# Performance work log

Hardware: AMD Instinct MI355X
Metric: run time of the kernel (lower is better)

The kernel has to match this reference:

```python
import jax, jax.numpy as jnp
import numpy as np

T_MAX = 0.3  # clamp ceiling for effective opacity (t_max init kwarg)


def setup_inputs() -> dict:
    key = jax.random.key(0)
    k0, k1, k2 = jax.random.split(key, 3)
    B, n_blobs, d_s, d_f = 1024, 131072, 64, 256
    return {
        "query": jax.random.normal(k0, (B, d_s), dtype=jnp.float32),
        "mu": jax.random.normal(k1, (n_blobs, d_s), dtype=jnp.float32) * 0.02,
        "log_var": jnp.zeros((n_blobs, d_s), dtype=jnp.float32),
        "raw_alpha": jnp.zeros((n_blobs,), dtype=jnp.float32),
        "features": jax.random.normal(k2, (n_blobs, d_f), dtype=jnp.float32) * 0.02,
        "log_tau": jnp.asarray(np.log(128.0), dtype=jnp.float32),
        "k": 16,
    }


def reference(query, mu, log_var, raw_alpha, features, log_tau, k):
    # query: [B, d_s]; mu/log_var: [N, d_s]; features: [N, d_f]
    tau = jnp.exp(log_tau)
    inv_var = jnp.exp(-log_var)                              # [N, d_s]
    # Mahalanobis distance expanded to avoid the [B, N, d_s] diff tensor:
    # sum_d (q - mu)^2 * iv = q^2.iv - 2 q.(mu*iv) + sum(mu^2*iv)
    q2 = jnp.einsum('bd,nd->bn', query * query, inv_var)      # [B, N]
    cross = jnp.einsum('bd,nd->bn', query, mu * inv_var)      # [B, N]
    m2 = jnp.sum(mu * mu * inv_var, axis=-1)                  # [N]
    mahal = q2 - 2.0 * cross + m2[None, :]
    K_all = jnp.exp(-0.5 * mahal / tau)                       # [B, N]
    alpha = jax.nn.sigmoid(raw_alpha)                         # [N]
    scores = K_all * alpha[None, :]
    top_scores, top_idx = jax.lax.top_k(scores, k)            # [B, k]

    # Gather selected blobs and recompute exact kernel (as in the original render)
    blob_feats = features[top_idx]                            # [B, k, d_f]
    blob_mu = mu[top_idx]                                     # [B, k, d_s]
    blob_iv = jnp.exp(-log_var[top_idx])                      # [B, k, d_s]
    diff = query[:, None, :] - blob_mu                        # [B, k, d_s]
    mahal_k = jnp.sum(diff * diff * blob_iv, axis=-1)         # [B, k]
    K_topk = jnp.exp(-0.5 * mahal_k / tau)
    blob_alpha = alpha[top_idx]                               # [B, k]

    # Alpha compositing in log space
    eff = jnp.minimum(blob_alpha * K_topk, T_MAX / k)         # [B, k]
    log_1m = jnp.log1p(-jnp.minimum(eff, 1.0 - 1e-6))
    log_cum = jnp.cumsum(log_1m, axis=-1)
    log_T = jnp.concatenate(
        [jnp.zeros_like(log_cum[:, :1]), log_cum[:, :-1]], axis=-1)
    weights = eff * jnp.exp(log_T)                            # [B, k]
    blob_meaning = jnp.einsum('bk,bkd->bd', weights, blob_feats)  # [B, d_f]
    t_residual = jnp.exp(log_cum[:, -1])                      # [B]
    return blob_meaning, t_residual
```

## Files before the change

kernel.cpp:

```cpp
#include <hip/hip_runtime.h>
#include <math.h>

#define BQ    1024
#define NB    131072
#define DS    64
#define DF    256
#define KSEL  16

#define QT    128
#define BC    64
#define PCH   64
#define NCHUNK (NB / BC)
#define CHUNKS_PER_BLK (NCHUNK/PCH)
#define CPQ   (PCH * KSEL)
#define SLD   68

#define CH_BYTES   32768
#define SPLIT_OFF  16384

typedef __bf16 bf16x8 __attribute__((ext_vector_type(8)));
typedef float  f32x4  __attribute__((ext_vector_type(4)));
typedef unsigned long long u64;

__device__ __forceinline__ unsigned map_f32(float s) {
    unsigned u = __float_as_uint(s);
    return (u & 0x80000000u) ? ~u : (u | 0x80000000u);
}

__device__ __forceinline__ void async_cp16(const void* g, void* l) {
    __builtin_amdgcn_global_load_lds(
        (const __attribute__((address_space(1))) unsigned int*)g,
        (__attribute__((address_space(3))) unsigned int*)l, 16, 0, 0);
}

__global__ __launch_bounds__(256)
void prep_kernel(const float* __restrict__ mu,
                 const float* __restrict__ log_var,
                 const float* __restrict__ raw_alpha,
                 char* __restrict__ bprep,
                 float* __restrict__ m2la)
{
    int gid  = blockIdx.x * 256 + threadIdx.x;
    int blob = gid >> 3;
    int dd   = gid & 7;

    const float* mrow = mu      + (size_t)blob * DS + dd * 8;
    const float* vrow = log_var + (size_t)blob * DS + dd * 8;
    float4 ma = ((const float4*)mrow)[0], mb = ((const float4*)mrow)[1];
    float4 va = ((const float4*)vrow)[0], vb = ((const float4*)vrow)[1];
    float m[8] = {ma.x, ma.y, ma.z, ma.w, mb.x, mb.y, mb.z, mb.w};
    float lv[8] = {va.x, va.y, va.z, va.w, vb.x, vb.y, vb.z, vb.w};

    bf16x8 hiv, liv, hmv, lmv;
    float p = 0.0f;
    #pragma unroll
    for (int j = 0; j < 8; ++j) {
        float iv = __expf(-lv[j]);
        float mv = m[j] * iv;
        p += m[j] * mv;
        __bf16 h1 = (__bf16)iv;  hiv[j] = h1; liv[j] = (__bf16)(iv - (float)h1);
        __bf16 h2 = (__bf16)mv;  hmv[j] = h2; lmv[j] = (__bf16)(mv - (float)h2);
    }
    p += __shfl_xor(p, 1);
    p += __shfl_xor(p, 2);
    p += __shfl_xor(p, 4);

    int c  = blob >> 6;
    int nt = (blob >> 4) & 3;
    int bl = blob & 15;
    int lane  = (dd & 3) * 16 + bl;
    int ks_iv = dd >> 2;
    int ks_mv = 2 + (dd >> 2);
    size_t b_iv = (size_t)c * CH_BYTES + nt * 4096 + ks_iv * 1024 + lane * 16;
    size_t b_mv = (size_t)c * CH_BYTES + nt * 4096 + ks_mv * 1024 + lane * 16;
    *(bf16x8*)(bprep + b_iv)             = hiv;
    *(bf16x8*)(bprep + b_iv + SPLIT_OFF) = liv;
    *(bf16x8*)(bprep + b_mv)             = hmv;
    *(bf16x8*)(bprep + b_mv + SPLIT_OFF) = lmv;

    if (dd == 0) {
        m2la[blob * 2]     = p;
        m2la[blob * 2 + 1] = -log1pf(__expf(-raw_alpha[blob]));
    }
}

__device__ __forceinline__ void ins16(float (&ts)[16], int (&ti)[16],
                                      float& mymin, float s, int idx)
{
    float v0[8]; int j0[8];
    #pragma unroll
    for (int i = 0; i < 8; ++i) {
        bool b = ts[2*i+1] < ts[2*i];
        v0[i] = b ? ts[2*i+1] : ts[2*i];
        j0[i] = (i << 1) | (b ? 1 : 0);
    }
    float v1[4]; int j1[4];
    #pragma unroll
    for (int i = 0; i < 4; ++i) {
        bool b = v0[2*i+1] < v0[2*i];
        v1[i] = b ? v0[2*i+1] : v0[2*i];
        j1[i] = b ? j0[2*i+1] : j0[2*i];
    }
    float v2[2]; int j2[2];
    #pragma unroll
    for (int i = 0; i < 2; ++i) {
        bool b = v1[2*i+1] < v1[2*i];
        v2[i] = b ? v1[2*i+1] : v1[2*i];
        j2[i] = b ? j1[2*i+1] : j1[2*i];
    }
    int am = (v2[1] < v2[0]) ? j2[1] : j2[0];
    #pragma unroll
    for (int i = 0; i < 16; ++i) {
        bool b = (i == am);
        ts[i] = b ? s : ts[i];
        ti[i] = b ? idx : ti[i];
    }
    float n0[8];
    #pragma unroll
    for (int i = 0; i < 8; ++i) n0[i] = fminf(ts[2*i], ts[2*i+1]);
    float n1[4];
    #pragma unroll
    for (int i = 0; i < 4; ++i) n1[i] = fminf(n0[2*i], n0[2*i+1]);
    mymin = fminf(fminf(n1[0], n1[1]), fminf(n1[2], n1[3]));
}

__global__ __launch_bounds__(256, 2)
void score_topk_kernel(const float* __restrict__ query,
                       const char* __restrict__ bprep,
                       const float* __restrict__ m2la,
                       const float* __restrict__ log_tau_p,
                       u64* __restrict__ cand)
{
    __shared__ __align__(16) short Bs[CH_BYTES / 2];
    __shared__ __align__(16) float St[QT * SLD];
    __shared__ float scv[2 * QT];

    const int tid   = threadIdx.x;
    const int lane  = tid & 63;
    const int quad  = lane >> 4;
    const int mrow  = lane & 15;
    const int wv    = tid >> 6;
    const int qbase = blockIdx.y * QT;

    const float nhit = -0.5f * expf(-log_tau_p[0]);

    bf16x8 ahi[2][4], alo[2][4];
    #pragma unroll
    for (int mt = 0; mt < 2; ++mt) {
        const float* qrow = query + (size_t)(qbase + wv * 32 + mt * 16 + mrow) * DS;
        #pragma unroll
        for (int ks = 0; ks < 4; ++ks) {
            int kq = ks * 32 + quad * 8;
            int d0 = kq & 63;
            bool lin = kq >= 64;
            bf16x8 h, l;
            #pragma unroll
            for (int j = 0; j < 8; ++j) {
                float v = qrow[d0 + j];
                float x = lin ? (-2.0f * v) : (v * v);
                __bf16 hb = (__bf16)x;
                h[j] = hb;
                l[j] = (__bf16)(x - (float)hb);
            }
            ahi[mt][ks] = h; alo[mt][ks] = l;
        }
    }

    float ts[16]; int ti[16];
    #pragma unroll
    for (int i = 0; i < 16; ++i) { ts[i] = -INFINITY; ti[i] = 0; }
    float mymin = -INFINITY;
    const int qloc = tid & 127;
    const int half = tid >> 7;
    if (tid < 2 * QT) scv[tid] = -INFINITY;

    const char* BsB = (const char*)Bs;

    int c = blockIdx.x;
    {
        const char* src = bprep + (size_t)c * CH_BYTES;
        #pragma unroll
        for (int i = 0; i < 8; ++i) {
            int s = tid + i * 256;
            async_cp16(src + s * 16, (void*)(BsB + s * 16));
        }
    }
    __syncthreads();

    for (int it = 0; it < CHUNKS_PER_BLK; ++it) {
        const int nbase = c * BC;
        const int cn    = c + PCH;
        const bool more = (it + 1) < CHUNKS_PER_BLK;

        float2 ml[4];
        #pragma unroll
        for (int nt = 0; nt < 4; ++nt)
            ml[nt] = *(const float2*)&m2la[(size_t)(nbase + nt * 16 + mrow) * 2];

        f32x4 acc[2][4];
        #pragma unroll
        for (int nt = 0; nt < 4; ++nt) {
            bf16x8 bh[4], bl[4];
            #pragma unroll
            for (int ks = 0; ks < 4; ++ks) {
                bh[ks] = *(const bf16x8*)(BsB + nt * 4096 + ks * 1024 + lane * 16);
                bl[ks] = *(const bf16x8*)(BsB + SPLIT_OFF + nt * 4096 + ks * 1024 + lane * 16);
            }
            #pragma unroll
            for (int mt = 0; mt < 2; ++mt) {
                f32x4 a = {0.0f, 0.0f, 0.0f, 0.0f};
                #pragma unroll
                for (int ks = 0; ks < 4; ++ks) {
                    a = __builtin_amdgcn_mfma_f32_16x16x32_bf16(ahi[mt][ks], bh[ks], a, 0, 0, 0);
                    a = __builtin_amdgcn_mfma_f32_16x16x32_bf16(ahi[mt][ks], bl[ks], a, 0, 0, 0);
                    a = __builtin_amdgcn_mfma_f32_16x16x32_bf16(alo[mt][ks], bh[ks], a, 0, 0, 0);
                }
                acc[mt][nt] = a;
            }
        }
        __syncthreads();

        if (more) {
            const char* src = bprep + (size_t)cn * CH_BYTES;
            #pragma unroll
            for (int i = 0; i < 8; ++i) {
                int s = tid + i * 256;
                async_cp16(src + s * 16, (void*)(BsB + s * 16));
            }
        }

        #pragma unroll
        for (int mt = 0; mt < 2; ++mt)
            #pragma unroll
            for (int nt = 0; nt < 4; ++nt) {
                float m2 = ml[nt].x, la = ml[nt].y;
                #pragma unroll
                for (int reg = 0; reg < 4; ++reg) {
                    float sc = nhit * (acc[mt][nt][reg] + m2) + la;
                    St[(wv * 32 + mt * 16 + quad * 4 + reg) * SLD + nt * 16 + mrow] = sc;
                }
            }
        __syncthreads();

        {
            volatile float* vsc = scv;
            float ocut = vsc[(half ^ 1) * QT + qloc];
            float cut = fmaxf(mymin, ocut);
            const float* rowp = &St[qloc * SLD + half * 32];
            unsigned gm = 0u;
            #pragma unroll
            for (int i = 0; i < 8; ++i) {
                float4 v = ((const float4*)rowp)[i];
                float mx = fmaxf(fmaxf(v.x, v.y), fmaxf(v.z, v.w));
                if (mx > cut) gm |= (1u << i);
            }
            while (__any(gm != 0u)) {
                if (gm) {
                    int i = __ffs(gm) - 1;
                    gm &= gm - 1u;
                    float4 v = ((const float4*)rowp)[i];
                    int b0 = nbase + half * 32 + i * 4;
                    if (v.x > cut) { ins16(ts, ti, mymin, v.x, b0);     cut = fmaxf(mymin, ocut); }
                    if (v.y > cut) { ins16(ts, ti, mymin, v.y, b0 + 1); cut = fmaxf(mymin, ocut); }
                    if (v.z > cut) { ins16(ts, ti, mymin, v.z, b0 + 2); cut = fmaxf(mymin, ocut); }
                    if (v.w > cut) { ins16(ts, ti, mymin, v.w, b0 + 3); cut = fmaxf(mymin, ocut); }
                }
            }
            vsc[half * QT + qloc] = mymin;
        }
        __syncthreads();
        c = cn;
    }
    __syncthreads();

    u64* SK = (u64*)St;
    #pragma unroll
    for (int i = 0; i < 16; ++i)
        SK[qloc * 33 + half * 16 + i] =
            ((u64)map_f32(ts[i]) << 32) | (u64)(0xFFFFFFFFu - (unsigned)ti[i]);
    __syncthreads();

    if (tid < QT) {
        u64* row = SK + tid * 33;
        u64* dst = cand + (size_t)(qbase + tid) * CPQ + blockIdx.x * KSEL;
        for (int r = 0; r < KSEL; ++r) {
            int bm = 0; u64 bv = row[0];
            #pragma unroll 4
            for (int j = 1; j < 32; ++j) { u64 v = row[j]; if (v > bv) { bv = v; bm = j; } }
            row[bm] = 0;
            dst[r] = bv;
        }
    }
}

__global__ __launch_bounds__(256)
void merge_composite_kernel(const float* __restrict__ query,
                            const float* __restrict__ mu,
                            const float* __restrict__ log_var,
                            const float* __restrict__ raw_alpha,
                            const float* __restrict__ features,
                            const float* __restrict__ log_tau_p,
                            const u64* __restrict__ cand,
                            float* __restrict__ out)
{
    const int q   = blockIdx.x;
    const int tid = threadIdx.x;
    const int wv = tid >> 6, lane = tid & 63;

    __shared__ u64   wtop[4 * KSEL];
    __shared__ int   sel[KSEL];
    __shared__ float w_sh[KSEL];
    __shared__ float mah[KSEL];
    __shared__ float alp[KSEL];

    u64 k[4];
    #pragma unroll
    for (int r = 0; r < 4; ++r)
        k[r] = cand[(size_t)q * CPQ + wv * 256 + r * 64 + lane];

    for (int r = 0; r < KSEL; ++r) {
        u64 m = k[0];
        #pragma unroll
        for (int j = 1; j < 4; ++j) if (k[j] > m) m = k[j];
        #pragma unroll
        for (int off = 32; off > 0; off >>= 1) {
            unsigned hi = __shfl_xor((unsigned)(m >> 32), off);
            unsigned lo = __shfl_xor((unsigned)(m & 0xFFFFFFFFu), off);
            u64 o = ((u64)hi << 32) | lo;
            if (o > m) m = o;
        }
        if (lane == 0) wtop[wv * KSEL + r] = m;
        #pragma unroll
        for (int j = 0; j < 4; ++j) if (k[j] == m) k[j] = 0ull;
    }
    __syncthreads();

    if (wv == 0) {
        u64 kk = wtop[lane];
        for (int r = 0; r < KSEL; ++r) {
            u64 m = kk;
            #pragma unroll
            for (int off = 32; off > 0; off >>= 1) {
                unsigned hi = __shfl_xor((unsigned)(m >> 32), off);
                unsigned lo = __shfl_xor((unsigned)(m & 0xFFFFFFFFu), off);
                u64 o = ((u64)hi << 32) | lo;
                if (o > m) m = o;
            }
            if (kk == m) kk = 0ull;
            if (lane == 0)
                sel[r] = (int)(0xFFFFFFFFu - (unsigned)(m & 0xFFFFFFFFull));
        }
    }
    __syncthreads();

    for (int r = wv; r < KSEL; r += 4) {
        int bi = sel[r];
        float qd = query[(size_t)q * DS + lane];
        float mv = mu[(size_t)bi * DS + lane];
        float d  = qd - mv;
        float t  = d * d * expf(-log_var[(size_t)bi * DS + lane]);
        #pragma unroll
        for (int off = 32; off > 0; off >>= 1) t += __shfl_down(t, off);
        if (lane == 0) {
            mah[r] = t;
            alp[r] = 1.0f / (1.0f + expf(-raw_alpha[bi]));
        }
    }
    __syncthreads();

    if (tid == 0) {
        float tau = expf(log_tau_p[0]);
        float cap = 0.3f / 16.0f;
        float logT = 0.0f;
        for (int r = 0; r < KSEL; ++r) {
            float K   = expf(-0.5f * mah[r] / tau);
            float eff = fminf(alp[r] * K, cap);
            w_sh[r]   = eff * expf(logT);
            logT     += log1pf(-fminf(eff, 1.0f - 1e-6f));
        }
        out[(size_t)BQ * DF + q] = expf(logT);
    }
    __syncthreads();

    {
        float a = 0.0f;
        #pragma unroll
        for (int r = 0; r < KSEL; ++r)
            a += w_sh[r] * features[(size_t)sel[r] * DF + tid];
        out[(size_t)q * DF + tid] = a;
    }
}

extern "C" void kernel_launch(void* const* d_in, const int* in_sizes, int n_in,
                              void* d_out, int out_size, void* d_ws, size_t ws_size,
                              hipStream_t stream)
{
    (void)in_sizes; (void)n_in; (void)out_size; (void)ws_size;
    const float* query     = (const float*)d_in[0];
    const float* mu        = (const float*)d_in[1];
    const float* log_var   = (const float*)d_in[2];
    const float* raw_alpha = (const float*)d_in[3];
    const float* features  = (const float*)d_in[4];
    const float* log_tau   = (const float*)d_in[5];
    float* out = (float*)d_out;

    char*  bprep = (char*)d_ws;
    float* m2la  = (float*)((char*)d_ws + (size_t)NCHUNK * CH_BYTES);
    u64*   cand  = (u64*)((char*)d_ws + (size_t)NCHUNK * CH_BYTES + (size_t)NB * 2 * 4);

    prep_kernel<<<(NB * 8) / 256, 256, 0, stream>>>(mu, log_var, raw_alpha, bprep, m2la);

    dim3 g2(PCH, BQ / QT);
    score_topk_kernel<<<g2, 256, 0, stream>>>(query, bprep, m2la, log_tau, cand);

    merge_composite_kernel<<<BQ, 256, 0, stream>>>(query, mu, log_var, raw_alpha,
                                                   features, log_tau, cand, out);
}
```

Baseline: 659.1 us.

## Share per-query top-k cutoff across blocks via global atomicMax

Each thread publishes its current 16th-best score to a per-query global slot with atomicMax once per chunk. It reads back the largest cutoff seen across all blocks and uses it to prune candidate insertions into its local top-16 list. This is meant to cut time spent in the divergent insertion loop during early chunks, when local thresholds are still low. It adds one global atomic per thread per chunk, uses the output's t_residual region as scratch (initialised in prep_kernel and overwritten later by the merge kernel), and relies on the order-preserving float encoding.

```diff
diff --git a/kernel.cpp b/kernel.cpp
--- a/kernel.cpp
+++ b/kernel.cpp
@@ -22,9 +22,15 @@
 typedef float  f32x4  __attribute__((ext_vector_type(4)));
 typedef unsigned long long u64;
 
+#define ENC_NEGINF 0x007FFFFFu
+
 __device__ __forceinline__ unsigned map_f32(float s) {
     unsigned u = __float_as_uint(s);
     return (u & 0x80000000u) ? ~u : (u | 0x80000000u);
+}
+
+__device__ __forceinline__ float unmap_f32(unsigned e) {
+    return __uint_as_float((e & 0x80000000u) ? (e & 0x7FFFFFFFu) : ~e);
 }
 
 __device__ __forceinline__ void async_cp16(const void* g, void* l) {
@@ -38,9 +44,11 @@
                  const float* __restrict__ log_var,
                  const float* __restrict__ raw_alpha,
                  char* __restrict__ bprep,
-                 float* __restrict__ m2la)
+                 float* __restrict__ m2la,
+                 unsigned* __restrict__ gcut)
 {
     int gid  = blockIdx.x * 256 + threadIdx.x;
+    if (gid < BQ) gcut[gid] = ENC_NEGINF;
     int blob = gid >> 3;
     int dd   = gid & 7;
 
@@ -129,7 +137,8 @@
                        const char* __restrict__ bprep,
                        const float* __restrict__ m2la,
                        const float* __restrict__ log_tau_p,
-                       u64* __restrict__ cand)
+                       u64* __restrict__ cand,
+                       unsigned* __restrict__ gcut)
 {
     __shared__ __align__(16) short Bs[CH_BYTES / 2];
     __shared__ __align__(16) float St[QT * SLD];
@@ -173,6 +182,7 @@
     const int qloc = tid & 127;
     const int half = tid >> 7;
     if (tid < 2 * QT) scv[tid] = -INFINITY;
+    unsigned* const gslot = gcut + qbase + qloc;
 
     const char* BsB = (const char*)Bs;
 
@@ -191,6 +201,8 @@
         const int nbase = c * BC;
         const int cn    = c + PCH;
         const bool more = (it + 1) < CHUNKS_PER_BLK;
+
+        unsigned eg = atomicMax(gslot, map_f32(mymin));
 
         float2 ml[4];
         #pragma unroll
@@ -245,7 +257,9 @@
         {
             volatile float* vsc = scv;
             float ocut = vsc[(half ^ 1) * QT + qloc];
-            float cut = fmaxf(mymin, ocut);
+            float gc   = unmap_f32(eg);
+            float bcut = fmaxf(ocut, gc);
+            float cut  = fmaxf(mymin, bcut);
             const float* rowp = &St[qloc * SLD + half * 32];
             unsigned gm = 0u;
             #pragma unroll
@@ -260,10 +274,10 @@
                     gm &= gm - 1u;
                     float4 v = ((const float4*)rowp)[i];
                     int b0 = nbase + half * 32 + i * 4;
-                    if (v.x > cut) { ins16(ts, ti, mymin, v.x, b0);     cut = fmaxf(mymin, ocut); }
-                    if (v.y > cut) { ins16(ts, ti, mymin, v.y, b0 + 1); cut = fmaxf(mymin, ocut); }
-                    if (v.z > cut) { ins16(ts, ti, mymin, v.z, b0 + 2); cut = fmaxf(mymin, ocut); }
-                    if (v.w > cut) { ins16(ts, ti, mymin, v.w, b0 + 3); cut = fmaxf(mymin, ocut); }
+                    if (v.x > cut) { ins16(ts, ti, mymin, v.x, b0);     cut = fmaxf(mymin, bcut); }
+                    if (v.y > cut) { ins16(ts, ti, mymin, v.y, b0 + 1); cut = fmaxf(mymin, bcut); }
+                    if (v.z > cut) { ins16(ts, ti, mymin, v.z, b0 + 2); cut = fmaxf(mymin, bcut); }
+                    if (v.w > cut) { ins16(ts, ti, mymin, v.w, b0 + 3); cut = fmaxf(mymin, bcut); }
                 }
             }
             vsc[half * QT + qloc] = mymin;
@@ -407,11 +421,12 @@
     char*  bprep = (char*)d_ws;
     float* m2la  = (float*)((char*)d_ws + (size_t)NCHUNK * CH_BYTES);
     u64*   cand  = (u64*)((char*)d_ws + (size_t)NCHUNK * CH_BYTES + (size_t)NB * 2 * 4);
-
-    prep_kernel<<<(NB * 8) / 256, 256, 0, stream>>>(mu, log_var, raw_alpha, bprep, m2la);
+    unsigned* gcut = (unsigned*)(out + (size_t)BQ * DF);
+
+    prep_kernel<<<(NB * 8) / 256, 256, 0, stream>>>(mu, log_var, raw_alpha, bprep, m2la, gcut);
 
     dim3 g2(PCH, BQ / QT);
-    score_topk_kernel<<<g2, 256, 0, stream>>>(query, bprep, m2la, log_tau, cand);
+    score_topk_kernel<<<g2, 256, 0, stream>>>(query, bprep, m2la, log_tau, cand, gcut);
 
     merge_composite_kernel<<<BQ, 256, 0, stream>>>(query, mu, log_var, raw_alpha,
                                                    features, log_tau, cand, out);
```

Measured after the change: 602.3 us. 8.6% less time.
